# Performance work log

Measured on AMD Instinct MI355X. Metric: run time of the kernel, lower is better.

The kernel has to match this reference:

```python
import jax, jax.numpy as jnp
import numpy as np

D_MODEL = 4096
NUM_HEADS = 32
D_K = D_MODEL // NUM_HEADS  # 128
SEQ = D_K  # module's final `O @ scores` requires h*seq == O.shape[1] == d_model -> seq == d_k
WSCALE = 0.02


def setup_inputs() -> dict:
    key = jax.random.key(0)
    kq, kk, kv, ko, kx = jax.random.split(key, 5)
    Q = jax.random.normal(kq, (D_MODEL, D_MODEL), jnp.float32) * WSCALE
    K = jax.random.normal(kk, (D_MODEL, D_MODEL), jnp.float32) * WSCALE
    V = jax.random.normal(kv, (D_MODEL, D_MODEL), jnp.float32) * WSCALE
    O = jax.random.normal(ko, (D_MODEL, D_MODEL), jnp.float32) * WSCALE
    x = jax.random.normal(kx, (SEQ, D_MODEL), jnp.float32)
    return {"Q": Q, "K": K, "V": V, "O": O, "x": x}


def reference(Q, K, V, O, x):
    h, d = NUM_HEADS, D_K
    seq = x.shape[0]
    # stack and split weights into per-head projections: (3, h, d, d_in)
    qkv_w = jnp.stack((Q, K, V), axis=0).reshape(3, h, d, -1)
    # project: (3, h, seq, d)
    proj = jnp.einsum('phdi,si->phsd', qkv_w, x)
    q_proj, k_proj, v_proj = proj[0], proj[1], proj[2]
    # attention scores: (h, seq, seq)
    scores = jnp.einsum('hqd,hkd->hqk', q_proj, k_proj) / jnp.sqrt(jnp.asarray(d, scores_dtype := q_proj.dtype))
    # module uses triu (upper-triangular incl. diagonal) mask, multiply then fill zeros with -inf
    mask = jnp.triu(jnp.ones((seq, seq), dtype=scores.dtype))
    masked = mask * scores
    masked = jnp.where(masked == 0.0, -jnp.inf, masked)
    # stable softmax over keys (single exp, same math as subtract-max softmax)
    shifted = masked - jnp.max(masked, axis=-1, keepdims=True)
    e = jnp.exp(shifted)
    probs = e / jnp.sum(e, axis=-1, keepdims=True)
    # attention output: (h, seq, d)
    att = jnp.einsum('hqk,hkd->hqd', probs, v_proj)
    # module flattens (h, seq) together: ((h*seq), d), then left-multiplies by O
    att = att.reshape(h * seq, d)
    return O @ att  # (d_model, d_k)
```

## Files before the change

kernel.cpp:

```cpp
#include <hip/hip_runtime.h>
#include <stdint.h>

#define DM 4096

typedef __attribute__((ext_vector_type(4))) float f32x4;
typedef __attribute__((ext_vector_type(8))) short s16x8;
typedef __attribute__((ext_vector_type(8))) unsigned short u16x8;
typedef __attribute__((ext_vector_type(4))) unsigned short u16x4;

__device__ __forceinline__ unsigned short f2bf(float f) {
  union { float f; unsigned u; } c; c.f = f;
  unsigned u = c.u;
  u += 0x7FFFu + ((u >> 16) & 1u);
  return (unsigned short)(u >> 16);
}
__device__ __forceinline__ float bf2f(unsigned short h) {
  union { unsigned u; float f; } c; c.u = ((unsigned)h) << 16;
  return c.f;
}

__device__ __forceinline__ void splitbf(float v, short& hi, short& lo) {
  union { float f; unsigned u; } c; c.f = v;
  unsigned uh = c.u & 0xFFFF0000u;
  hi = (short)(uh >> 16);
  union { unsigned u; float f; } d; d.u = uh;
  lo = (short)f2bf(v - d.f);
}

__global__ __launch_bounds__(256) void k0_xsplit(const float* __restrict__ x,
                                                 unsigned short* __restrict__ xh) {
  int g = blockIdx.x * 256 + threadIdx.x;
  int kg = g & 511, s = g >> 9;
  const float* px = x + (size_t)s * DM + kg * 8;
  f32x4 v0 = *(const f32x4*)px;
  f32x4 v1 = *(const f32x4*)(px + 4);
  u16x8 hi;
#pragma unroll
  for (int j = 0; j < 8; ++j) {
    float v = (j < 4) ? v0[j] : v1[j - 4];
    hi[j] = f2bf(v);
  }
  *(u16x8*)(xh + ((size_t)kg * 128 + s) * 8) = hi;
}

__global__ __launch_bounds__(256) void k1_proj(const float* __restrict__ Q,
                                               const float* __restrict__ K,
                                               const float* __restrict__ V,
                                               const unsigned short* __restrict__ xh,
                                               float* __restrict__ pp) {
  __shared__ __align__(16) unsigned short xs[4096];
  int bid = blockIdx.x;
  int rb = bid >> 1, kc = bid & 1;
  int r0 = rb * 64;
  int w = r0 >> 12;
  int rloc = r0 & 4095;
  const float* W = (w == 0) ? Q : ((w == 1) ? K : V);
  int tid = threadIdx.x;
  int wave = tid >> 6, lane = tid & 63;
  int l15 = lane & 15, lg = lane >> 4;
  int rwb = rloc + wave * 16;
  const float* arow = W + (size_t)(rwb + l15) * DM + lg * 8;
  int kbase = kc * 2048;
  f32x4 acc[8];
#pragma unroll
  for (int i = 0; i < 8; ++i) acc[i] = (f32x4)0.f;

  u16x8 xA[2], xB[2];
  f32x4 aA[2], aB[2];
  auto loadx = [&](u16x8* xb, int kk) {
    const u16x8* s = (const u16x8*)(xh + (size_t)kk * 128);
    xb[0] = s[tid];
    xb[1] = s[256 + tid];
  };
  auto loada = [&](f32x4* ab, int kk) {
    ab[0] = *(const f32x4*)(arow + kk);
    ab[1] = *(const f32x4*)(arow + kk + 4);
  };
  loadx(xA, kbase);      loada(aA, kbase);
  loadx(xB, kbase + 32); loada(aB, kbase + 32);

  auto step = [&](u16x8* xb, f32x4* ab, int kkp) {
    __syncthreads();
    ((u16x8*)xs)[tid] = xb[0];
    ((u16x8*)xs)[256 + tid] = xb[1];
    s16x8 Ahi, Alo;
#pragma unroll
    for (int j = 0; j < 8; ++j) {
      float v = (j < 4) ? ab[0][j] : ab[1][j - 4];
      short h, l; splitbf(v, h, l);
      Ahi[j] = h; Alo[j] = l;
    }
    loadx(xb, kkp);
    loada(ab, kkp);
    __syncthreads();
#pragma unroll
    for (int nt = 0; nt < 8; ++nt) {
      s16x8 bh = *(const s16x8*)&xs[((lg * 128) + nt * 16 + l15) * 8];
      acc[nt] = __builtin_amdgcn_mfma_f32_16x16x32_bf16(Ahi, bh, acc[nt], 0, 0, 0);
      acc[nt] = __builtin_amdgcn_mfma_f32_16x16x32_bf16(Alo, bh, acc[nt], 0, 0, 0);
    }
  };

  for (int t = 0; t < 64; t += 2) {
    int kk0 = kbase + t * 32;
    step(xA, aA, (t + 2 < 64) ? kk0 + 64 : kk0);
    step(xB, aB, (t + 3 < 64) ? kk0 + 96 : kk0 + 32);
  }

  int h = rwb >> 7;
  int dbase = (rwb & 127) + (lg << 2);
  size_t base = (size_t)(kc * 3 + w) * 524288;
  if (w < 2) {
#pragma unroll
    for (int nt = 0; nt < 8; ++nt) {
      int s = nt * 16 + l15;
      *(f32x4*)(pp + base + (size_t)(h * 128 + s) * 128 + dbase) = acc[nt];
    }
  } else {
#pragma unroll
    for (int nt = 0; nt < 8; ++nt) {
      int s = nt * 16 + l15;
#pragma unroll
      for (int r = 0; r < 4; ++r)
        pp[base + (size_t)(h * 128 + dbase + r) * 128 + s] = acc[nt][r];
    }
  }
}

__global__ __launch_bounds__(256) void k2_attn(const float* __restrict__ pp,
                                               unsigned short* __restrict__ att) {
  __shared__ __align__(16) unsigned short lds[32768];
  int h = blockIdx.x;
  int tid = threadIdx.x, wave = tid >> 6, lane = tid & 63;
  int l15 = lane & 15, lg = lane >> 4;
  const float* pk0 = pp + (size_t)1 * 524288 + (size_t)h * 16384;
  const float* pk1 = pp + (size_t)4 * 524288 + (size_t)h * 16384;
  const float* pv0 = pp + (size_t)2 * 524288 + (size_t)h * 16384;
  const float* pv1 = pp + (size_t)5 * 524288 + (size_t)h * 16384;
  for (int g = tid; g < 2048; g += 256) {
    int dg = g & 15, k = g >> 4;
    size_t so = (size_t)k * 128 + dg * 8;
    f32x4 u0 = *(const f32x4*)(pk0 + so);
    f32x4 u1 = *(const f32x4*)(pk0 + so + 4);
    f32x4 w0 = *(const f32x4*)(pk1 + so);
    f32x4 w1 = *(const f32x4*)(pk1 + so + 4);
    u16x8 kb;
#pragma unroll
    for (int j = 0; j < 4; ++j) {
      kb[j] = f2bf(u0[j] + w0[j]);
      kb[4 + j] = f2bf(u1[j] + w1[j]);
    }
    *(u16x8*)&lds[(size_t)(dg * 128 + k) * 8] = kb;
    int kg = g & 15, d = g >> 4;
    size_t vo = (size_t)d * 128 + kg * 8;
    f32x4 x0 = *(const f32x4*)(pv0 + vo);
    f32x4 x1 = *(const f32x4*)(pv0 + vo + 4);
    f32x4 y0 = *(const f32x4*)(pv1 + vo);
    f32x4 y1 = *(const f32x4*)(pv1 + vo + 4);
    u16x8 vb;
#pragma unroll
    for (int j = 0; j < 4; ++j) {
      vb[j] = f2bf(x0[j] + y0[j]);
      vb[4 + j] = f2bf(x1[j] + y1[j]);
    }
    *(u16x8*)&lds[16384 + (size_t)(kg * 128 + d) * 8] = vb;
  }
  __syncthreads();

  int qbase = wave * 32;
  const float* pq0 = pp + (size_t)h * 16384;
  const float* pq1 = pp + (size_t)3 * 524288 + (size_t)h * 16384;
  const float RS = 0.08838834764831845f;
  f32x4 sc[2][8];
#pragma unroll
  for (int a = 0; a < 2; ++a)
#pragma unroll
    for (int b = 0; b < 8; ++b) sc[a][b] = (f32x4)0.f;

  for (int ks = 0; ks < 4; ++ks) {
    s16x8 qhi[2], qlo[2];
#pragma unroll
    for (int qt = 0; qt < 2; ++qt) {
      int q = qbase + qt * 16 + l15;
      size_t qo = (size_t)q * 128 + ks * 32 + lg * 8;
      f32x4 u0 = *(const f32x4*)(pq0 + qo);
      f32x4 u1 = *(const f32x4*)(pq0 + qo + 4);
      f32x4 w0 = *(const f32x4*)(pq1 + qo);
      f32x4 w1 = *(const f32x4*)(pq1 + qo + 4);
#pragma unroll
      for (int j = 0; j < 8; ++j) {
        float v = ((j < 4) ? (u0[j] + w0[j]) : (u1[j - 4] + w1[j - 4])) * RS;
        unsigned short hh = f2bf(v);
        qhi[qt][j] = (short)hh;
        qlo[qt][j] = (short)f2bf(v - bf2f(hh));
      }
    }
#pragma unroll
    for (int nt = 0; nt < 8; ++nt) {
      s16x8 kb = *(const s16x8*)&lds[(size_t)((ks * 4 + lg) * 128 + nt * 16 + l15) * 8];
#pragma unroll
      for (int qt = 0; qt < 2; ++qt) {
        sc[qt][nt] = __builtin_amdgcn_mfma_f32_16x16x32_bf16(qhi[qt], kb, sc[qt][nt], 0, 0, 0);
        sc[qt][nt] = __builtin_amdgcn_mfma_f32_16x16x32_bf16(qlo[qt], kb, sc[qt][nt], 0, 0, 0);
      }
    }
  }
  float inv[2][4];
#pragma unroll
  for (int qt = 0; qt < 2; ++qt) {
#pragma unroll
    for (int r = 0; r < 4; ++r) {
      int q = qbase + qt * 16 + (lg << 2) + r;
      float m = -3.0e38f;
#pragma unroll
      for (int nt = 0; nt < 8; ++nt) {
        int k = nt * 16 + l15;
        float v = sc[qt][nt][r];
        if (k >= q) m = fmaxf(m, v);
      }
#pragma unroll
      for (int d = 1; d < 16; d <<= 1) m = fmaxf(m, __shfl_xor(m, d));
      float ssum = 0.f;
#pragma unroll
      for (int nt = 0; nt < 8; ++nt) {
        int k = nt * 16 + l15;
        float v = sc[qt][nt][r];
        float e = (k >= q) ? __expf(v - m) : 0.f;
        sc[qt][nt][r] = e;
        ssum += e;
      }
#pragma unroll
      for (int d = 1; d < 16; d <<= 1) ssum += __shfl_xor(ssum, d);
      inv[qt][r] = 1.f / ssum;
    }
  }
  __syncthreads();
#pragma unroll
  for (int qt = 0; qt < 2; ++qt)
#pragma unroll
    for (int nt = 0; nt < 8; ++nt) {
      int k = nt * 16 + l15;
#pragma unroll
      for (int r = 0; r < 4; ++r) {
        int q = qbase + qt * 16 + (lg << 2) + r;
        lds[(size_t)((k >> 3) * 128 + q) * 8 + (k & 7)] = f2bf(sc[qt][nt][r] * inv[qt][r]);
      }
    }
  __syncthreads();
  f32x4 o[2][8];
#pragma unroll
  for (int a = 0; a < 2; ++a)
#pragma unroll
    for (int b = 0; b < 8; ++b) o[a][b] = (f32x4)0.f;
  for (int ks = 0; ks < 4; ++ks) {
    s16x8 pa[2];
#pragma unroll
    for (int qt = 0; qt < 2; ++qt)
      pa[qt] = *(const s16x8*)&lds[(size_t)((ks * 4 + lg) * 128 + qbase + qt * 16 + l15) * 8];
#pragma unroll
    for (int nt = 0; nt < 8; ++nt) {
      s16x8 vb = *(const s16x8*)&lds[16384 + (size_t)((ks * 4 + lg) * 128 + nt * 16 + l15) * 8];
      o[0][nt] = __builtin_amdgcn_mfma_f32_16x16x32_bf16(pa[0], vb, o[0][nt], 0, 0, 0);
      o[1][nt] = __builtin_amdgcn_mfma_f32_16x16x32_bf16(pa[1], vb, o[1][nt], 0, 0, 0);
    }
  }
#pragma unroll
  for (int qt = 0; qt < 2; ++qt)
#pragma unroll
    for (int nt = 0; nt < 8; ++nt) {
      int d = nt * 16 + l15;
      int q = qbase + qt * 16 + (lg << 2);
      size_t j = (size_t)h * 128 + q;
      u16x4 pk;
#pragma unroll
      for (int r = 0; r < 4; ++r) pk[r] = f2bf(o[qt][nt][r]);
      *(u16x4*)(att + (size_t)d * DM + j) = pk;
    }
}

__global__ __launch_bounds__(256) void k3_out(const float* __restrict__ O,
                                              const unsigned short* __restrict__ att,
                                              float* __restrict__ out) {
  int bid = blockIdx.x;
  int rb = bid >> 2, kc = bid & 3;
  int r0 = rb * 16;
  int kbase = kc * 1024;
  int tid = threadIdx.x, wave = tid >> 6, lane = tid & 63;
  int l15 = lane & 15, lg = lane >> 4;
  const float* arow = O + (size_t)(r0 + l15) * DM + lg * 8;
  int c0 = wave * 32;
  const unsigned short* b0p = att + (size_t)(c0 + l15) * DM + lg * 8;
  const unsigned short* b1p = att + (size_t)(c0 + 16 + l15) * DM + lg * 8;
  f32x4 acc0 = (f32x4)0.f, acc1 = (f32x4)0.f;

  f32x4 aA[2], aB[2];
  s16x8 bA0, bA1, bB0, bB1;
  auto load = [&](f32x4* ab, s16x8& b0, s16x8& b1, int j0) {
    ab[0] = *(const f32x4*)(arow + j0);
    ab[1] = *(const f32x4*)(arow + j0 + 4);
    b0 = *(const s16x8*)(b0p + j0);
    b1 = *(const s16x8*)(b1p + j0);
  };
  load(aA, bA0, bA1, kbase);
  load(aB, bB0, bB1, kbase + 32);

  auto step = [&](f32x4* ab, s16x8& b0, s16x8& b1, int j0p) {
    s16x8 Ahi, Alo;
#pragma unroll
    for (int j = 0; j < 8; ++j) {
      float v = (j < 4) ? ab[0][j] : ab[1][j - 4];
      short h, l; splitbf(v, h, l);
      Ahi[j] = h; Alo[j] = l;
    }
    s16x8 v0 = b0, v1 = b1;
    load(ab, b0, b1, j0p);
    acc0 = __builtin_amdgcn_mfma_f32_16x16x32_bf16(Ahi, v0, acc0, 0, 0, 0);
    acc0 = __builtin_amdgcn_mfma_f32_16x16x32_bf16(Alo, v0, acc0, 0, 0, 0);
    acc1 = __builtin_amdgcn_mfma_f32_16x16x32_bf16(Ahi, v1, acc1, 0, 0, 0);
    acc1 = __builtin_amdgcn_mfma_f32_16x16x32_bf16(Alo, v1, acc1, 0, 0, 0);
  };

  for (int t = 0; t < 32; t += 2) {
    int j0 = kbase + t * 32;
    step(aA, bA0, bA1, (t + 2 < 32) ? j0 + 64 : j0);
    step(aB, bB0, bB1, (t + 3 < 32) ? j0 + 96 : j0 + 32);
  }
#pragma unroll
  for (int r = 0; r < 4; ++r) {
    int row = r0 + (lg << 2) + r;
    atomicAdd(&out[(size_t)row * 128 + c0 + l15], acc0[r]);
    atomicAdd(&out[(size_t)row * 128 + c0 + 16 + l15], acc1[r]);
  }
}

extern "C" void kernel_launch(void* const* d_in, const int* in_sizes, int n_in,
                              void* d_out, int out_size, void* d_ws, size_t ws_size,
                              hipStream_t stream) {
  const float* Q = (const float*)d_in[0];
  const float* K = (const float*)d_in[1];
  const float* V = (const float*)d_in[2];
  const float* O = (const float*)d_in[3];
  const float* x = (const float*)d_in[4];
  float* out = (float*)d_out;
  uint8_t* ws = (uint8_t*)d_ws;
  unsigned short* xh = (unsigned short*)ws;
  unsigned short* att = (unsigned short*)(ws + (1u << 20));
  float* pp = (float*)(ws + (2u << 20));
  hipMemsetAsync(d_out, 0, (size_t)out_size * sizeof(float), stream);
  hipLaunchKernelGGL(k0_xsplit, dim3(256), dim3(256), 0, stream, x, xh);
  hipLaunchKernelGGL(k1_proj, dim3(384), dim3(256), 0, stream, Q, K, V, xh, pp);
  hipLaunchKernelGGL(k2_attn, dim3(32), dim3(256), 0, stream, pp, att);
  hipLaunchKernelGGL(k3_out, dim3(1024), dim3(256), 0, stream, O, att, out);
}
```

Measured before the change: 318.8 us.

## Deepen prefetch to four stages and restructure output GEMM with LDS-staged att

The projection kernel now keeps four k-steps of loads in flight in registers instead of two. It also swaps __syncthreads for a lighter s_barrier that waits only on lgkmcnt, so outstanding global loads no longer stall the barrier. The attention kernel writes att in a k-blocked interleaved layout. The output kernel now mirrors the projection kernel: 64-row tiles, att chunks staged in LDS, eight accumulators per wave, 512 blocks over 8 k-splits. The costs are higher register pressure, more atomics per block, and the correctness of a barrier that does not wait on vmcnt before the LDS stores.

```diff
diff --git a/kernel.cpp b/kernel.cpp
--- a/kernel.cpp
+++ b/kernel.cpp
@@ -25,6 +25,11 @@
   hi = (short)(uh >> 16);
   union { unsigned u; float f; } d; d.u = uh;
   lo = (short)f2bf(v - d.f);
+}
+
+__device__ __forceinline__ void wave_barrier_lgkm() {
+  asm volatile("s_waitcnt lgkmcnt(0)" ::: "memory");
+  __builtin_amdgcn_s_barrier();
 }
 
 __global__ __launch_bounds__(256) void k0_xsplit(const float* __restrict__ x,
@@ -65,46 +70,49 @@
 #pragma unroll
   for (int i = 0; i < 8; ++i) acc[i] = (f32x4)0.f;
 
-  u16x8 xA[2], xB[2];
-  f32x4 aA[2], aB[2];
-  auto loadx = [&](u16x8* xb, int kk) {
+  u16x8 xb[4][2];
+  f32x4 ab[4][2];
+#pragma unroll
+  for (int p = 0; p < 4; ++p) {
+    int kk = kbase + p * 32;
     const u16x8* s = (const u16x8*)(xh + (size_t)kk * 128);
-    xb[0] = s[tid];
-    xb[1] = s[256 + tid];
-  };
-  auto loada = [&](f32x4* ab, int kk) {
-    ab[0] = *(const f32x4*)(arow + kk);
-    ab[1] = *(const f32x4*)(arow + kk + 4);
-  };
-  loadx(xA, kbase);      loada(aA, kbase);
-  loadx(xB, kbase + 32); loada(aB, kbase + 32);
-
-  auto step = [&](u16x8* xb, f32x4* ab, int kkp) {
-    __syncthreads();
-    ((u16x8*)xs)[tid] = xb[0];
-    ((u16x8*)xs)[256 + tid] = xb[1];
-    s16x8 Ahi, Alo;
-#pragma unroll
-    for (int j = 0; j < 8; ++j) {
-      float v = (j < 4) ? ab[0][j] : ab[1][j - 4];
-      short h, l; splitbf(v, h, l);
-      Ahi[j] = h; Alo[j] = l;
-    }
-    loadx(xb, kkp);
-    loada(ab, kkp);
-    __syncthreads();
-#pragma unroll
-    for (int nt = 0; nt < 8; ++nt) {
-      s16x8 bh = *(const s16x8*)&xs[((lg * 128) + nt * 16 + l15) * 8];
-      acc[nt] = __builtin_amdgcn_mfma_f32_16x16x32_bf16(Ahi, bh, acc[nt], 0, 0, 0);
-      acc[nt] = __builtin_amdgcn_mfma_f32_16x16x32_bf16(Alo, bh, acc[nt], 0, 0, 0);
-    }
-  };
-
-  for (int t = 0; t < 64; t += 2) {
-    int kk0 = kbase + t * 32;
-    step(xA, aA, (t + 2 < 64) ? kk0 + 64 : kk0);
-    step(xB, aB, (t + 3 < 64) ? kk0 + 96 : kk0 + 32);
+    xb[p][0] = s[tid];
+    xb[p][1] = s[256 + tid];
+    ab[p][0] = *(const f32x4*)(arow + kk);
+    ab[p][1] = *(const f32x4*)(arow + kk + 4);
+  }
+
+  for (int tt = 0; tt < 16; ++tt) {
+#pragma unroll
+    for (int p = 0; p < 4; ++p) {
+      int t = tt * 4 + p;
+      wave_barrier_lgkm();
+      ((u16x8*)xs)[tid] = xb[p][0];
+      ((u16x8*)xs)[256 + tid] = xb[p][1];
+      s16x8 Ahi, Alo;
+#pragma unroll
+      for (int j = 0; j < 8; ++j) {
+        float v = (j < 4) ? ab[p][0][j] : ab[p][1][j - 4];
+        short h, l; splitbf(v, h, l);
+        Ahi[j] = h; Alo[j] = l;
+      }
+      int tp = t + 4;
+      int kkp = kbase + ((tp < 64) ? tp : 0) * 32;
+      {
+        const u16x8* s = (const u16x8*)(xh + (size_t)kkp * 128);
+        xb[p][0] = s[tid];
+        xb[p][1] = s[256 + tid];
+        ab[p][0] = *(const f32x4*)(arow + kkp);
+        ab[p][1] = *(const f32x4*)(arow + kkp + 4);
+      }
+      wave_barrier_lgkm();
+#pragma unroll
+      for (int nt = 0; nt < 8; ++nt) {
+        s16x8 bh = *(const s16x8*)&xs[((lg * 128) + nt * 16 + l15) * 8];
+        acc[nt] = __builtin_amdgcn_mfma_f32_16x16x32_bf16(Ahi, bh, acc[nt], 0, 0, 0);
+        acc[nt] = __builtin_amdgcn_mfma_f32_16x16x32_bf16(Alo, bh, acc[nt], 0, 0, 0);
+      }
+    }
   }
 
   int h = rwb >> 7;
@@ -268,68 +276,82 @@
   for (int qt = 0; qt < 2; ++qt)
 #pragma unroll
     for (int nt = 0; nt < 8; ++nt) {
-      int d = nt * 16 + l15;
-      int q = qbase + qt * 16 + (lg << 2);
-      size_t j = (size_t)h * 128 + q;
+      int c = nt * 16 + l15;
+      int jq = h * 128 + qbase + qt * 16 + (lg << 2);
       u16x4 pk;
 #pragma unroll
       for (int r = 0; r < 4; ++r) pk[r] = f2bf(o[qt][nt][r]);
-      *(u16x4*)(att + (size_t)d * DM + j) = pk;
+      *(u16x4*)(att + (size_t)(jq >> 3) * 1024 + c * 8 + (jq & 7)) = pk;
     }
 }
 
 __global__ __launch_bounds__(256) void k3_out(const float* __restrict__ O,
                                               const unsigned short* __restrict__ att,
                                               float* __restrict__ out) {
+  __shared__ __align__(16) unsigned short ats[4096];
   int bid = blockIdx.x;
-  int rb = bid >> 2, kc = bid & 3;
-  int r0 = rb * 16;
-  int kbase = kc * 1024;
+  int rb = bid >> 3, kc = bid & 7;
+  int r0 = rb * 64;
+  int kbase = kc * 512;
   int tid = threadIdx.x, wave = tid >> 6, lane = tid & 63;
   int l15 = lane & 15, lg = lane >> 4;
-  const float* arow = O + (size_t)(r0 + l15) * DM + lg * 8;
-  int c0 = wave * 32;
-  const unsigned short* b0p = att + (size_t)(c0 + l15) * DM + lg * 8;
-  const unsigned short* b1p = att + (size_t)(c0 + 16 + l15) * DM + lg * 8;
-  f32x4 acc0 = (f32x4)0.f, acc1 = (f32x4)0.f;
-
-  f32x4 aA[2], aB[2];
-  s16x8 bA0, bA1, bB0, bB1;
-  auto load = [&](f32x4* ab, s16x8& b0, s16x8& b1, int j0) {
-    ab[0] = *(const f32x4*)(arow + j0);
-    ab[1] = *(const f32x4*)(arow + j0 + 4);
-    b0 = *(const s16x8*)(b0p + j0);
-    b1 = *(const s16x8*)(b1p + j0);
-  };
-  load(aA, bA0, bA1, kbase);
-  load(aB, bB0, bB1, kbase + 32);
-
-  auto step = [&](f32x4* ab, s16x8& b0, s16x8& b1, int j0p) {
-    s16x8 Ahi, Alo;
-#pragma unroll
-    for (int j = 0; j < 8; ++j) {
-      float v = (j < 4) ? ab[0][j] : ab[1][j - 4];
-      short h, l; splitbf(v, h, l);
-      Ahi[j] = h; Alo[j] = l;
-    }
-    s16x8 v0 = b0, v1 = b1;
-    load(ab, b0, b1, j0p);
-    acc0 = __builtin_amdgcn_mfma_f32_16x16x32_bf16(Ahi, v0, acc0, 0, 0, 0);
-    acc0 = __builtin_amdgcn_mfma_f32_16x16x32_bf16(Alo, v0, acc0, 0, 0, 0);
-    acc1 = __builtin_amdgcn_mfma_f32_16x16x32_bf16(Ahi, v1, acc1, 0, 0, 0);
-    acc1 = __builtin_amdgcn_mfma_f32_16x16x32_bf16(Alo, v1, acc1, 0, 0, 0);
-  };
-
-  for (int t = 0; t < 32; t += 2) {
-    int j0 = kbase + t * 32;
-    step(aA, bA0, bA1, (t + 2 < 32) ? j0 + 64 : j0);
-    step(aB, bB0, bB1, (t + 3 < 32) ? j0 + 96 : j0 + 32);
-  }
-#pragma unroll
-  for (int r = 0; r < 4; ++r) {
-    int row = r0 + (lg << 2) + r;
-    atomicAdd(&out[(size_t)row * 128 + c0 + l15], acc0[r]);
-    atomicAdd(&out[(size_t)row * 128 + c0 + 16 + l15], acc1[r]);
+  int rwb = r0 + wave * 16;
+  const float* arow = O + (size_t)(rwb + l15) * DM + lg * 8;
+  f32x4 acc[8];
+#pragma unroll
+  for (int i = 0; i < 8; ++i) acc[i] = (f32x4)0.f;
+
+  u16x8 bb[4][2];
+  f32x4 ab[4][2];
+#pragma unroll
+  for (int p = 0; p < 4; ++p) {
+    int kk = kbase + p * 32;
+    const u16x8* s = (const u16x8*)(att + (size_t)(kk >> 3) * 1024);
+    bb[p][0] = s[tid];
+    bb[p][1] = s[256 + tid];
+    ab[p][0] = *(const f32x4*)(arow + kk);
+    ab[p][1] = *(const f32x4*)(arow + kk + 4);
+  }
+
+  for (int tt = 0; tt < 4; ++tt) {
+#pragma unroll
+    for (int p = 0; p < 4; ++p) {
+      int t = tt * 4 + p;
+      wave_barrier_lgkm();
+      ((u16x8*)ats)[tid] = bb[p][0];
+      ((u16x8*)ats)[256 + tid] = bb[p][1];
+      s16x8 Ahi, Alo;
+#pragma unroll
+      for (int j = 0; j < 8; ++j) {
+        float v = (j < 4) ? ab[p][0][j] : ab[p][1][j - 4];
+        short h, l; splitbf(v, h, l);
+        Ahi[j] = h; Alo[j] = l;
+      }
+      int tp = t + 4;
+      int kkp = kbase + ((tp < 16) ? tp : 0) * 32;
+      {
+        const u16x8* s = (const u16x8*)(att + (size_t)(kkp >> 3) * 1024);
+        bb[p][0] = s[tid];
+        bb[p][1] = s[256 + tid];
+        ab[p][0] = *(const f32x4*)(arow + kkp);
+        ab[p][1] = *(const f32x4*)(arow + kkp + 4);
+      }
+      wave_barrier_lgkm();
+#pragma unroll
+      for (int nt = 0; nt < 8; ++nt) {
+        s16x8 bh = *(const s16x8*)&ats[((lg * 128) + nt * 16 + l15) * 8];
+        acc[nt] = __builtin_amdgcn_mfma_f32_16x16x32_bf16(Ahi, bh, acc[nt], 0, 0, 0);
+        acc[nt] = __builtin_amdgcn_mfma_f32_16x16x32_bf16(Alo, bh, acc[nt], 0, 0, 0);
+      }
+    }
+  }
+#pragma unroll
+  for (int nt = 0; nt < 8; ++nt) {
+#pragma unroll
+    for (int r = 0; r < 4; ++r) {
+      int row = rwb + (lg << 2) + r;
+      atomicAdd(&out[(size_t)row * 128 + nt * 16 + l15], acc[nt][r]);
+    }
   }
 }
 
@@ -350,5 +372,5 @@
   hipLaunchKernelGGL(k0_xsplit, dim3(256), dim3(256), 0, stream, x, xh);
   hipLaunchKernelGGL(k1_proj, dim3(384), dim3(256), 0, stream, Q, K, V, xh, pp);
   hipLaunchKernelGGL(k2_attn, dim3(32), dim3(256), 0, stream, pp, att);
-  hipLaunchKernelGGL(k3_out, dim3(1024), dim3(256), 0, stream, O, att, out);
-}
+  hipLaunchKernelGGL(k3_out, dim3(512), dim3(256), 0, stream, O, att, out);
+}
```

After: 288.5 us. -9.5%, faster.
